# Kernel optimization log

Measured on AMD Instinct MI355X. Metric: run time of the kernel, lower is better.

The kernel has to match this reference:

```python
import jax, jax.numpy as jnp
import numpy as np
from jax import lax

T = 2048          # sequential steps (the torch 'batch' loop)
N = 32768         # n_neurons
TAU_M = 20.0
V_THRESH = 1.0
V_RESET = 0.0
ALPHA = float(np.exp(-1.0 / TAU_M))
BETA = 1.0 - ALPHA


def setup_inputs() -> dict:
    key = jax.random.key(0)
    currents = jax.random.normal(key, (T, N), dtype=jnp.float32)
    v0 = jnp.zeros((N,), dtype=jnp.float32)  # initial membrane voltage buffer
    return {"currents": currents, "v0": v0}


def reference(currents, v0):
    """LIF decay -> threshold -> reset recurrence over T steps.

    Returns (spikes, voltages), each of shape (T, N), matching the torch
    module's stacked per-step outputs (post-reset voltages).
    """
    alpha = jnp.float32(ALPHA)
    beta = jnp.float32(BETA)

    def step(v, c):
        v = alpha * v + beta * c                      # leaky integration
        s = (v >= V_THRESH).astype(jnp.float32)       # spike (binary)
        v = v * (1.0 - s) + V_RESET * s               # reset where spiked
        return v, (s, v)

    _, (spikes, voltages) = lax.scan(step, v0, currents)
    return spikes, voltages
```

## Files before the change

kernel.cpp:

```cpp
#include <hip/hip_runtime.h>


constexpr int T_STEPS = 2048;
constexpr int N_NEUR  = 32768;
constexpr int CHUNK   = 512;
constexpr int WARM    = 160;
constexpr int UNROLL  = 8;

__global__ __launch_bounds__(256) void lif_chunked(
    const float* __restrict__ cur, const float* __restrict__ v0,
    float* __restrict__ out)
{
    const float ALPHA = (float)0.95122942450071400909;
    const float BETA  = (float)(1.0 - 0.95122942450071400909);

    const int n     = blockIdx.x * blockDim.x + threadIdx.x;
    const int chunk = blockIdx.y;
    const int t0    = chunk * CHUNK;

    float* __restrict__ spikes = out;
    float* __restrict__ volts  = out + (size_t)T_STEPS * N_NEUR;

    float v;
    int   nwarm;
    if (chunk == 0) { v = v0[n]; nwarm = 0; }
    else            { v = 0.0f;  nwarm = WARM; }

    const float* p = cur + (size_t)(t0 - nwarm) * N_NEUR + n;

    for (int t = 0; t < nwarm; t += UNROLL) {
        float c[UNROLL];
        #pragma unroll
        for (int i = 0; i < UNROLL; ++i) c[i] = p[(size_t)i * N_NEUR];
        #pragma unroll
        for (int i = 0; i < UNROLL; ++i) {
            v = ALPHA * v + BETA * c[i];
            v = (v >= 1.0f) ? 0.0f : v;
        }
        p += (size_t)UNROLL * N_NEUR;
    }

    float buf[UNROLL];
    #pragma unroll
    for (int i = 0; i < UNROLL; ++i) buf[i] = p[(size_t)i * N_NEUR];

    constexpr int G = CHUNK / UNROLL;
    size_t idx = (size_t)t0 * N_NEUR + n;
    for (int g = 0; g < G; ++g) {
        float nxt[UNROLL];
        const bool more = (g + 1 < G);
        if (more) {
            const float* q = p + (size_t)UNROLL * N_NEUR;
            #pragma unroll
            for (int i = 0; i < UNROLL; ++i) nxt[i] = q[(size_t)i * N_NEUR];
        }
        #pragma unroll
        for (int i = 0; i < UNROLL; ++i) {
            v = ALPHA * v + BETA * buf[i];
            float s = (v >= 1.0f) ? 1.0f : 0.0f;
            v       = (v >= 1.0f) ? 0.0f : v;
            spikes[idx] = s;
            volts[idx]  = v;
            idx += N_NEUR;
        }
        if (more) {
            #pragma unroll
            for (int i = 0; i < UNROLL; ++i) buf[i] = nxt[i];
            p += (size_t)UNROLL * N_NEUR;
        }
    }
}

extern "C" void kernel_launch(void* const* d_in, const int* in_sizes, int n_in,
                              void* d_out, int out_size, void* d_ws, size_t ws_size,
                              hipStream_t stream) {
    const float* cur = (const float*)d_in[0];
    const float* v0  = (const float*)d_in[1];
    float* out = (float*)d_out;

    dim3 block(256);
    dim3 grid(N_NEUR / 256, T_STEPS / CHUNK);
    lif_chunked<<<grid, block, 0, stream>>>(cur, v0, out);
}
```

Baseline: 707.1 us.

## Vectorize LIF neurons as float2, add nontemporal stores and double-buffered loads

Each thread now handles two adjacent neurons using 8-byte float2 loads and stores, which halves the neuron-dimension grid. The time dimension is split into more chunks (8 instead of 4), so the total block count stays the same while each block does shorter sequential work. Loads go through ping-pong A/B register buffers, and output writes use nontemporal stores to avoid polluting the cache. More chunks mean more redundant warm-up steps reading currents, and the wider per-thread state raises register use.

Result: no change. 712.8 us (+0.8%).

```diff
diff --git a/kernel.cpp b/kernel.cpp
--- a/kernel.cpp
+++ b/kernel.cpp
@@ -1,72 +1,99 @@
 #include <hip/hip_runtime.h>
 
 
+typedef float v2 __attribute__((ext_vector_type(2)));
+
 constexpr int T_STEPS = 2048;
 constexpr int N_NEUR  = 32768;
-constexpr int CHUNK   = 512;
+constexpr int N2      = N_NEUR / 2;
+constexpr int NCHUNK  = 8;
+constexpr int CHUNK   = T_STEPS / NCHUNK;
 constexpr int WARM    = 160;
-constexpr int UNROLL  = 8;
+constexpr int U       = 8;
 
-__global__ __launch_bounds__(256) void lif_chunked(
-    const float* __restrict__ cur, const float* __restrict__ v0,
-    float* __restrict__ out)
-{
+__device__ __forceinline__ void lif_step(v2& v, v2 c, v2& s) {
     const float ALPHA = (float)0.95122942450071400909;
     const float BETA  = (float)(1.0 - 0.95122942450071400909);
+    v = ALPHA * v + BETA * c;
+    s.x = (v.x >= 1.0f) ? 1.0f : 0.0f;
+    s.y = (v.y >= 1.0f) ? 1.0f : 0.0f;
+    v.x = (v.x >= 1.0f) ? 0.0f : v.x;
+    v.y = (v.y >= 1.0f) ? 0.0f : v.y;
+}
 
+__global__ __launch_bounds__(256) void lif_v2(
+    const v2* __restrict__ cur, const v2* __restrict__ v0,
+    v2* __restrict__ spikes, v2* __restrict__ volts)
+{
     const int n     = blockIdx.x * blockDim.x + threadIdx.x;
     const int chunk = blockIdx.y;
     const int t0    = chunk * CHUNK;
 
-    float* __restrict__ spikes = out;
-    float* __restrict__ volts  = out + (size_t)T_STEPS * N_NEUR;
+    v2 v;
+    v2 A[U], B[U];
 
-    float v;
-    int   nwarm;
-    if (chunk == 0) { v = v0[n]; nwarm = 0; }
-    else            { v = 0.0f;  nwarm = WARM; }
-
-    const float* p = cur + (size_t)(t0 - nwarm) * N_NEUR + n;
-
-    for (int t = 0; t < nwarm; t += UNROLL) {
-        float c[UNROLL];
+    if (chunk == 0) {
+        v = v0[n];
+    } else {
+        v.x = 0.0f; v.y = 0.0f;
+        const v2* q = cur + (size_t)(t0 - WARM) * N2 + n;
+        constexpr int GW = WARM / U;
         #pragma unroll
-        for (int i = 0; i < UNROLL; ++i) c[i] = p[(size_t)i * N_NEUR];
-        #pragma unroll
-        for (int i = 0; i < UNROLL; ++i) {
-            v = ALPHA * v + BETA * c[i];
-            v = (v >= 1.0f) ? 0.0f : v;
+        for (int i = 0; i < U; ++i) A[i] = q[(size_t)i * N2];
+        q += (size_t)U * N2;
+        for (int g = 0; g < GW; g += 2) {
+            if (g + 1 < GW) {
+                #pragma unroll
+                for (int i = 0; i < U; ++i) B[i] = q[(size_t)i * N2];
+                q += (size_t)U * N2;
+            }
+            v2 s;
+            #pragma unroll
+            for (int i = 0; i < U; ++i) lif_step(v, A[i], s);
+            if (g + 2 < GW) {
+                #pragma unroll
+                for (int i = 0; i < U; ++i) A[i] = q[(size_t)i * N2];
+                q += (size_t)U * N2;
+            }
+            if (g + 1 < GW) {
+                #pragma unroll
+                for (int i = 0; i < U; ++i) lif_step(v, B[i], s);
+            }
         }
-        p += (size_t)UNROLL * N_NEUR;
     }
 
-    float buf[UNROLL];
+    const v2* p = cur + (size_t)t0 * N2 + n;
+    size_t idx = (size_t)t0 * N2 + n;
+    constexpr int G = CHUNK / U;
+
     #pragma unroll
-    for (int i = 0; i < UNROLL; ++i) buf[i] = p[(size_t)i * N_NEUR];
+    for (int i = 0; i < U; ++i) A[i] = p[(size_t)i * N2];
+    p += (size_t)U * N2;
 
-    constexpr int G = CHUNK / UNROLL;
-    size_t idx = (size_t)t0 * N_NEUR + n;
-    for (int g = 0; g < G; ++g) {
-        float nxt[UNROLL];
-        const bool more = (g + 1 < G);
-        if (more) {
-            const float* q = p + (size_t)UNROLL * N_NEUR;
+    for (int g = 0; g < G; g += 2) {
+        #pragma unroll
+        for (int i = 0; i < U; ++i) B[i] = p[(size_t)i * N2];
+        p += (size_t)U * N2;
+        #pragma unroll
+        for (int i = 0; i < U; ++i) {
+            v2 s;
+            lif_step(v, A[i], s);
+            __builtin_nontemporal_store(s, &spikes[idx]);
+            __builtin_nontemporal_store(v, &volts[idx]);
+            idx += N2;
+        }
+        if (g + 2 < G) {
             #pragma unroll
-            for (int i = 0; i < UNROLL; ++i) nxt[i] = q[(size_t)i * N_NEUR];
+            for (int i = 0; i < U; ++i) A[i] = p[(size_t)i * N2];
+            p += (size_t)U * N2;
         }
         #pragma unroll
-        for (int i = 0; i < UNROLL; ++i) {
-            v = ALPHA * v + BETA * buf[i];
-            float s = (v >= 1.0f) ? 1.0f : 0.0f;
-            v       = (v >= 1.0f) ? 0.0f : v;
-            spikes[idx] = s;
-            volts[idx]  = v;
-            idx += N_NEUR;
-        }
-        if (more) {
-            #pragma unroll
-            for (int i = 0; i < UNROLL; ++i) buf[i] = nxt[i];
-            p += (size_t)UNROLL * N_NEUR;
+        for (int i = 0; i < U; ++i) {
+            v2 s;
+            lif_step(v, B[i], s);
+            __builtin_nontemporal_store(s, &spikes[idx]);
+            __builtin_nontemporal_store(v, &volts[idx]);
+            idx += N2;
         }
     }
 }
@@ -74,11 +101,12 @@
 extern "C" void kernel_launch(void* const* d_in, const int* in_sizes, int n_in,
                               void* d_out, int out_size, void* d_ws, size_t ws_size,
                               hipStream_t stream) {
-    const float* cur = (const float*)d_in[0];
-    const float* v0  = (const float*)d_in[1];
-    float* out = (float*)d_out;
+    const v2* cur = (const v2*)d_in[0];
+    const v2* v0  = (const v2*)d_in[1];
+    v2* spikes = (v2*)d_out;
+    v2* volts  = (v2*)d_out + (size_t)T_STEPS * N2;
 
     dim3 block(256);
-    dim3 grid(N_NEUR / 256, T_STEPS / CHUNK);
-    lif_chunked<<<grid, block, 0, stream>>>(cur, v0, out);
+    dim3 grid(N2 / 256, NCHUNK);
+    lif_v2<<<grid, block, 0, stream>>>(cur, v0, spikes, volts);
 }
```
